# Kernel tuning notes

Measured on AMD Instinct MI355X. Metric: run time of the kernel, lower is better.

The kernel has to match this reference:

```python
import jax, jax.numpy as jnp
import numpy as np
import math

N_HEADS = 16

def _layernorm(x, g, b):
    m = x.mean(-1, keepdims=True)
    v = ((x - m) ** 2).mean(-1, keepdims=True)
    return (x - m) * jax.lax.rsqrt(v + 1e-5) * g + b

def _project(x):
    # Poincare ball (c=1) projection: clip last-dim norm to 1 - eps
    max_norm = 1.0 - 1e-5
    n = jnp.linalg.norm(x, axis=-1, keepdims=True)
    return jnp.where(n > max_norm, x * (max_norm / jnp.maximum(n, 1e-12)), x)


def setup_inputs() -> dict:
    key = jax.random.key(0)
    ks = jax.random.split(key, 8)
    B, L, D = 2, 2048, 1024
    w = lambda k, s: jax.random.normal(k, s, jnp.float32) * 0.02
    return dict(
        x=jax.random.normal(ks[0], (B, L, D), jnp.float32),
        wq=w(ks[1], (D, D)), bq=jnp.zeros((D,), jnp.float32),
        wk=w(ks[2], (D, D)), bk=jnp.zeros((D,), jnp.float32),
        wv=w(ks[3], (D, D)), bv=jnp.zeros((D,), jnp.float32),
        wo=w(ks[4], (D, D)), bo=jnp.zeros((D,), jnp.float32),
        g1=jnp.ones((D,), jnp.float32), b1=jnp.zeros((D,), jnp.float32),
        g2=jnp.ones((D,), jnp.float32), b2=jnp.zeros((D,), jnp.float32),
        w1=w(ks[5], (4 * D, D)), bf1=jnp.zeros((4 * D,), jnp.float32),
        w2=w(ks[6], (D, 4 * D)), bf2=jnp.zeros((D,), jnp.float32),
    )


def reference(x, wq, bq, wk, bk, wv, bv, wo, bo, g1, b1, g2, b2, w1, bf1, w2, bf2):
    B, L, D = x.shape
    H = N_HEADS
    hd = D // H
    temp = math.sqrt(hd)

    xn = _layernorm(x, g1, b1)

    def heads(w, b):
        y = xn @ w.T + b                       # [B, L, D]
        return y.reshape(B, L, H, hd).transpose(0, 2, 1, 3)  # [B, H, L, hd]

    q = _project(heads(wq, bq))
    k = _project(heads(wk, bk))
    v = heads(wv, bv)

    # -||q - k||^2 / temp, via ||q||^2 + ||k||^2 - 2 q.k (same math as the
    # explicit broadcast-diff in the torch code, expressed as a GEMM)
    q2 = (q ** 2).sum(-1)[..., :, None]        # [B, H, L, 1]
    k2 = (k ** 2).sum(-1)[..., None, :]        # [B, H, 1, L]
    qk = jnp.einsum('bhld,bhmd->bhlm', q, k)   # [B, H, L, L]
    scores = -(q2 + k2 - 2.0 * qk) / temp
    attn = jax.nn.softmax(scores, axis=-1)     # dropout = identity (eval mode)

    out = jnp.einsum('bhlm,bhmd->bhld', attn, v)
    out = out.transpose(0, 2, 1, 3).reshape(B, L, D) @ wo.T + bo

    x = _project(x + out)
    xn2 = _layernorm(x, g2, b2)
    h = jax.nn.gelu(xn2 @ w1.T + bf1, approximate=False)  # torch nn.GELU = erf
    x = _project(x + (h @ w2.T + bf2))
    return x
```

## Files before the change

kernel.cpp:

```cpp
#include <hip/hip_runtime.h>
#include <math.h>

#define SEQ_L 2048
#define DM    1024
#define NH    16
#define HD    64
#define BL    4096
#define DFF   4096
#define QKV_S 3072

typedef __attribute__((ext_vector_type(8))) short short8;
typedef __attribute__((ext_vector_type(4))) short s16x4;
typedef __attribute__((ext_vector_type(4))) float f32x4;

#define AS1 __attribute__((address_space(1)))
#define AS3 __attribute__((address_space(3)))

__device__ __forceinline__ void gl_lds16(const void* g, void* l) {
    __builtin_amdgcn_global_load_lds((const AS1 void*)g, (AS3 void*)l, 16, 0, 0);
}

__device__ __forceinline__ short f2bf(float x) {
    unsigned u = __float_as_uint(x);
    u += 0x7fff + ((u >> 16) & 1);
    return (short)(u >> 16);
}
__device__ __forceinline__ float bf2f(short s) {
    return __uint_as_float(((unsigned)(unsigned short)s) << 16);
}

__device__ __forceinline__ float gelu_erf(float x) {
    return 0.5f * x * (1.f + erff(x * 0.70710678118654752440f));
}

__device__ __forceinline__ float block_sum(float v, float* red, int tid) {
#pragma unroll
    for (int m = 32; m; m >>= 1) v += __shfl_xor(v, m);
    if ((tid & 63) == 0) red[tid >> 6] = v;
    __syncthreads();
    v = red[0] + red[1] + red[2] + red[3];
    __syncthreads();
    return v;
}

__global__ __launch_bounds__(256) void cvt6_kernel(
    const float* __restrict__ wq, const float* __restrict__ wk,
    const float* __restrict__ wv, const float* __restrict__ wo,
    const float* __restrict__ w1, const float* __restrict__ w2,
    short* __restrict__ dst) {
    const size_t i = (size_t)blockIdx.x * 256 + threadIdx.x;
    const float* src;
    size_t off;
    if (i < 1048576) {
        const int seg = (int)(i >> 18);
        off = i & 262143;
        src = seg == 0 ? wq : seg == 1 ? wk : seg == 2 ? wv : wo;
    } else if (i < 2097152) { src = w1; off = i - 1048576; }
    else                    { src = w2; off = i - 2097152; }
    const float4 v = ((const float4*)src)[off];
    const s16x4 o = {f2bf(v.x), f2bf(v.y), f2bf(v.z), f2bf(v.w)};
    ((s16x4*)dst)[i] = o;
}

__global__ __launch_bounds__(256) void ln_bf16_kernel(const float* __restrict__ x,
                                                      const float* __restrict__ g,
                                                      const float* __restrict__ b,
                                                      short* __restrict__ out) {
    const int row = blockIdx.x;
    const int tid = threadIdx.x;
    __shared__ float red[4];
    const float4 xv = *(const float4*)(x + (size_t)row * DM + tid * 4);
    float s = xv.x + xv.y + xv.z + xv.w;
    s = block_sum(s, red, tid);
    const float mean = s * (1.f / (float)DM);
    float dx0 = xv.x - mean, dx1 = xv.y - mean, dx2 = xv.z - mean, dx3 = xv.w - mean;
    float ss = dx0 * dx0 + dx1 * dx1 + dx2 * dx2 + dx3 * dx3;
    ss = block_sum(ss, red, tid);
    const float rs = 1.f / sqrtf(ss * (1.f / (float)DM) + 1e-5f);
    const float4 gv = *(const float4*)(g + tid * 4);
    const float4 bv = *(const float4*)(b + tid * 4);
    const s16x4 ob = {f2bf(dx0 * rs * gv.x + bv.x), f2bf(dx1 * rs * gv.y + bv.y),
                      f2bf(dx2 * rs * gv.z + bv.z), f2bf(dx3 * rs * gv.w + bv.w)};
    *(s16x4*)(out + (size_t)row * DM + tid * 4) = ob;
}

__global__ __launch_bounds__(256) void resproj_kernel(const float* __restrict__ a,
                                                      const float* __restrict__ c,
                                                      float* __restrict__ out) {
    const int row = blockIdx.x;
    const int tid = threadIdx.x;
    __shared__ float red[4];
    const float4 av = *(const float4*)(a + (size_t)row * DM + tid * 4);
    const float4 cv = *(const float4*)(c + (size_t)row * DM + tid * 4);
    float4 sv;
    sv.x = av.x + cv.x; sv.y = av.y + cv.y; sv.z = av.z + cv.z; sv.w = av.w + cv.w;
    float ss = sv.x * sv.x + sv.y * sv.y + sv.z * sv.z + sv.w * sv.w;
    ss = block_sum(ss, red, tid);
    const float n = sqrtf(ss);
    const float mx = 1.f - 1e-5f;
    const float scale = (n > mx) ? (mx / fmaxf(n, 1e-12f)) : 1.f;
    sv.x *= scale; sv.y *= scale; sv.z *= scale; sv.w *= scale;
    *(float4*)(out + (size_t)row * DM + tid * 4) = sv;
}

__global__ __launch_bounds__(256) void qk_prep(const short* __restrict__ qkvB,
                                               short* __restrict__ Qb,
                                               short* __restrict__ Kb,
                                               float* __restrict__ k2) {
    const int tid = threadIdx.x, lane = tid & 63;
    const int vec = blockIdx.x * 4 + (tid >> 6);
    const int row = vec >> 4, h = vec & 15;
    const int b = row >> 11, l = row & 2047;
    const size_t dstv = ((size_t)(b * NH + h) * SEQ_L + l) * HD + lane;
    const float mx = 1.f - 1e-5f;
    {
        const float v = bf2f(qkvB[(size_t)row * QKV_S + h * HD + lane]);
        float s = v * v;
#pragma unroll
        for (int m = 32; m; m >>= 1) s += __shfl_xor(s, m);
        const float n = sqrtf(s);
        const float sc = (n > mx) ? (mx / fmaxf(n, 1e-12f)) : 1.f;
        Qb[dstv] = f2bf(v * sc);
    }
    {
        const float v = bf2f(qkvB[(size_t)row * QKV_S + DM + h * HD + lane]);
        float s = v * v;
#pragma unroll
        for (int m = 32; m; m >>= 1) s += __shfl_xor(s, m);
        const float n = sqrtf(s);
        const float sc = (n > mx) ? (mx / fmaxf(n, 1e-12f)) : 1.f;
        Kb[dstv] = f2bf(v * sc);
        if (lane == 0) k2[(size_t)(b * NH + h) * SEQ_L + l] = s * sc * sc * 0.125f;
    }
}

__global__ __launch_bounds__(256) void v_prep(const short* __restrict__ qkvB,
                                              short* __restrict__ Vtb) {
    const int blk = blockIdx.x;
    const int bh = blk >> 5, kt = blk & 31;
    const int b = bh >> 4, h = bh & 15;
    __shared__ short T[64 * 72];
    const int tid = threadIdx.x;
    {
        const int key = tid >> 2, ch = (tid & 3) * 16;
        const size_t src = ((size_t)b * SEQ_L + kt * 64 + key) * QKV_S + 2 * DM + h * HD + ch;
        *(short8*)&T[key * 72 + ch]     = *(const short8*)(qkvB + src);
        *(short8*)&T[key * 72 + ch + 8] = *(const short8*)(qkvB + src + 8);
    }
    __syncthreads();
    const int hd = tid >> 2, kc = (tid & 3) * 16;
    short8 o0, o1;
#pragma unroll
    for (int j = 0; j < 8; ++j) {
        o0[j] = T[(kc + j) * 72 + hd];
        o1[j] = T[(kc + 8 + j) * 72 + hd];
    }
    short* dst = Vtb + ((size_t)bh * HD + hd) * SEQ_L + kt * 64 + kc;
    *(short8*)dst = o0;
    *(short8*)(dst + 8) = o1;
}

template <int BM, int ACT, int OUTBF, int FUSED>
__global__ __launch_bounds__(256) void gemm_mfma(
    const short* __restrict__ A, const short* __restrict__ Bw,
    const float* __restrict__ bb0, const float* __restrict__ bb1,
    const float* __restrict__ bb2, void* __restrict__ Cout,
    int M, int N, int K) {
    constexpr int RT = BM / 32;
    __shared__ __align__(16) short As[BM * 32];
    __shared__ __align__(16) short Bs[128 * 32];
    const int tid = threadIdx.x;
    const int wv = tid >> 6, lane = tid & 63;
    const int m0 = blockIdx.y * BM, n0 = blockIdx.x * 128;
    const int wr = (wv & 1) * (BM / 2);
    const int wc = (wv >> 1) * 64;

    const int arow = wv * (BM / 4) + (lane >> 2);
    const int brow = wv * 32 + (lane >> 2);
    const short* Ag = A + (size_t)(m0 + arow) * K + (lane & 3) * 8;
    const short* Bg = Bw + (size_t)(n0 + brow) * K + (lane & 3) * 8;
    short* AsW = As + (wv * (BM / 4)) * 32;
    short* BsW = Bs + (wv * 32) * 32;

    const f32x4 z4 = {0.f, 0.f, 0.f, 0.f};
    f32x4 acc[RT][4];
#pragma unroll
    for (int r = 0; r < RT; ++r)
#pragma unroll
        for (int c = 0; c < 4; ++c) acc[r][c] = z4;

    const int lrow = lane & 15, kq = (lane >> 4) * 8;

    for (int kt = 0; kt < K; kt += 32) {
        __syncthreads();
        gl_lds16(Ag + kt, AsW);
        if constexpr (BM == 128) gl_lds16(Ag + (size_t)16 * K + kt, AsW + 16 * 32);
        gl_lds16(Bg + kt, BsW);
        gl_lds16(Bg + (size_t)16 * K + kt, BsW + 16 * 32);
        __syncthreads();
        short8 af[RT], bf[4];
#pragma unroll
        for (int r = 0; r < RT; ++r)
            af[r] = *(const short8*)&As[(wr + r * 16 + lrow) * 32 + kq];
#pragma unroll
        for (int c = 0; c < 4; ++c)
            bf[c] = *(const short8*)&Bs[(wc + c * 16 + lrow) * 32 + kq];
#pragma unroll
        for (int r = 0; r < RT; ++r)
#pragma unroll
            for (int c = 0; c < 4; ++c)
                acc[r][c] = __builtin_amdgcn_mfma_f32_16x16x32_bf16(af[r], bf[c], acc[r][c], 0, 0, 0);
    }

    const int col = lane & 15, rb = (lane >> 4) * 4;
#pragma unroll
    for (int c = 0; c < 4; ++c) {
        const int gn = n0 + wc + c * 16 + col;
        float bias;
        if constexpr (FUSED) {
            const int seg = gn >> 10;
            bias = (seg == 0 ? bb0 : seg == 1 ? bb1 : bb2)[gn & 1023];
        } else {
            bias = bb0[gn];
        }
#pragma unroll
        for (int r = 0; r < RT; ++r) {
            const int gm = m0 + wr + r * 16 + rb;
#pragma unroll
            for (int i = 0; i < 4; ++i) {
                float v = acc[r][c][i] + bias;
                if constexpr (ACT) v = gelu_erf(v);
                if constexpr (OUTBF)
                    ((short*)Cout)[(size_t)(gm + i) * N + gn] = f2bf(v);
                else
                    ((float*)Cout)[(size_t)(gm + i) * N + gn] = v;
            }
        }
    }
}

__global__ __launch_bounds__(256) void attn_mfma2(const short* __restrict__ Qb,
                                                  const short* __restrict__ Kb,
                                                  const short* __restrict__ Vtb,
                                                  const float* __restrict__ k2v,
                                                  short* __restrict__ aO) {
    const int qt = blockIdx.x, h = blockIdx.y, b = blockIdx.z;
    const int tid = threadIdx.x, wv = tid >> 6, lane = tid & 63;
    const int bh = b * NH + h;
    __shared__ __align__(16) short smem[2 * 64 * 72];
    short* Ks = smem;
    short* Vt = smem + 64 * 72;
    const int lrow = lane & 15, q8 = (lane >> 4) * 8, q4 = (lane >> 4) * 4;

    const short* Qh = Qb + (size_t)bh * SEQ_L * HD;
    const short* Kh = Kb + (size_t)bh * SEQ_L * HD;
    const short* Vh = Vtb + (size_t)bh * HD * SEQ_L;
    const float* k2p = k2v + (size_t)bh * SEQ_L;

    short8 qf[2][2];
#pragma unroll
    for (int nt = 0; nt < 2; ++nt)
#pragma unroll
        for (int kc = 0; kc < 2; ++kc)
            qf[nt][kc] = *(const short8*)(Qh +
                (size_t)(qt * 128 + wv * 32 + nt * 16 + lrow) * HD + kc * 32 + q8);

    const f32x4 z4 = {0.f, 0.f, 0.f, 0.f};
    f32x4 o[4][2];
#pragma unroll
    for (int ht = 0; ht < 4; ++ht)
#pragma unroll
        for (int nt = 0; nt < 2; ++nt) o[ht][nt] = z4;
    float lsum[2] = {0.f, 0.f};

    const int srow = tid >> 2, sch = (tid & 3) * 16;

    for (int kt = 0; kt < SEQ_L / 64; ++kt) {
        const int k0 = kt * 64;
        __syncthreads();
        {
            const short* g = Kh + (size_t)(k0 + srow) * HD + sch;
            *(short8*)&Ks[srow * 72 + sch]     = *(const short8*)g;
            *(short8*)&Ks[srow * 72 + sch + 8] = *(const short8*)(g + 8);
            const short* gv = Vh + (size_t)srow * SEQ_L + k0 + sch;
            *(short8*)&Vt[srow * 72 + sch]     = *(const short8*)gv;
            *(short8*)&Vt[srow * 72 + sch + 8] = *(const short8*)(gv + 8);
        }
        __syncthreads();

        short8 p8[2][2];
#pragma unroll
        for (int mt = 0; mt < 4; ++mt) {
            const short8 kf0 = *(const short8*)&Ks[(mt * 16 + lrow) * 72 + q8];
            const short8 kf1 = *(const short8*)&Ks[(mt * 16 + lrow) * 72 + 32 + q8];
            const float4 kk = *(const float4*)(k2p + k0 + mt * 16 + q4);
            const int c = mt >> 1, hi = (mt & 1) * 4;
#pragma unroll
            for (int nt = 0; nt < 2; ++nt) {
                f32x4 s = z4;
                s = __builtin_amdgcn_mfma_f32_16x16x32_bf16(kf0, qf[nt][0], s, 0, 0, 0);
                s = __builtin_amdgcn_mfma_f32_16x16x32_bf16(kf1, qf[nt][1], s, 0, 0, 0);
#pragma unroll
                for (int i = 0; i < 4; ++i) {
                    const float kki = (i == 0) ? kk.x : (i == 1) ? kk.y : (i == 2) ? kk.z : kk.w;
                    const float p = __expf(fmaf(s[i], 0.25f, -kki));
                    lsum[nt] += p;
                    p8[nt][c][hi + i] = f2bf(p);
                }
            }
        }
#pragma unroll
        for (int ht = 0; ht < 4; ++ht) {
#pragma unroll
            for (int c = 0; c < 2; ++c) {
                const s16x4 va = *(const s16x4*)&Vt[(ht * 16 + lrow) * 72 + c * 32 + q4];
                const s16x4 vb = *(const s16x4*)&Vt[(ht * 16 + lrow) * 72 + c * 32 + 16 + q4];
                const short8 v8 = {va[0], va[1], va[2], va[3], vb[0], vb[1], vb[2], vb[3]};
#pragma unroll
                for (int nt = 0; nt < 2; ++nt)
                    o[ht][nt] = __builtin_amdgcn_mfma_f32_16x16x32_bf16(v8, p8[nt][c], o[ht][nt], 0, 0, 0);
            }
        }
    }

#pragma unroll
    for (int nt = 0; nt < 2; ++nt) {
        lsum[nt] += __shfl_xor(lsum[nt], 16);
        lsum[nt] += __shfl_xor(lsum[nt], 32);
    }
    const float inv0 = 1.f / lsum[0], inv1 = 1.f / lsum[1];

    __syncthreads();
    short* Ot = smem + wv * (32 * 72);
#pragma unroll
    for (int ht = 0; ht < 4; ++ht)
#pragma unroll
        for (int nt = 0; nt < 2; ++nt) {
            const float iv = nt ? inv1 : inv0;
            const s16x4 ov = {f2bf(o[ht][nt][0] * iv), f2bf(o[ht][nt][1] * iv),
                              f2bf(o[ht][nt][2] * iv), f2bf(o[ht][nt][3] * iv)};
            *(s16x4*)&Ot[(nt * 16 + lrow) * 72 + ht * 16 + q4] = ov;
        }
    const int erow = lane >> 1, ec = (lane & 1) * 32;
    const short8 r0 = *(const short8*)&Ot[erow * 72 + ec + 0];
    const short8 r1 = *(const short8*)&Ot[erow * 72 + ec + 8];
    const short8 r2 = *(const short8*)&Ot[erow * 72 + ec + 16];
    const short8 r3 = *(const short8*)&Ot[erow * 72 + ec + 24];
    short* dst = aO + ((size_t)b * SEQ_L + qt * 128 + wv * 32 + erow) * DM + h * HD + ec;
    *(short8*)(dst + 0)  = r0;
    *(short8*)(dst + 8)  = r1;
    *(short8*)(dst + 16) = r2;
    *(short8*)(dst + 24) = r3;
}

extern "C" void kernel_launch(void* const* d_in, const int* in_sizes, int n_in,
                              void* d_out, int out_size, void* d_ws, size_t ws_size,
                              hipStream_t stream) {
    const float* x   = (const float*)d_in[0];
    const float* wq  = (const float*)d_in[1];
    const float* bq  = (const float*)d_in[2];
    const float* wk  = (const float*)d_in[3];
    const float* bk  = (const float*)d_in[4];
    const float* wv  = (const float*)d_in[5];
    const float* bv  = (const float*)d_in[6];
    const float* wo  = (const float*)d_in[7];
    const float* bo  = (const float*)d_in[8];
    const float* g1  = (const float*)d_in[9];
    const float* b1  = (const float*)d_in[10];
    const float* g2  = (const float*)d_in[11];
    const float* b2  = (const float*)d_in[12];
    const float* w1  = (const float*)d_in[13];
    const float* bf1 = (const float*)d_in[14];
    const float* w2  = (const float*)d_in[15];
    const float* bf2 = (const float*)d_in[16];
    float* out = (float*)d_out;

    char* base = (char*)d_ws;
    short* wbf  = (short*)base;
    short* qkvB = (short*)(base + (24u << 20));
    short* xnb  = (short*)(base + (48u << 20));
    short* Qb   = xnb;
    short* Kb   = (short*)(base + (56u << 20));
    short* Vtb  = (short*)(base + (64u << 20));
    float* k2   = (float*)(base + (72u << 20));
    short* aO   = (short*)(base + (72u << 20) + (256u << 10));
    float* P    = (float*)(base + (24u << 20));
    short* xn2b = Vtb;
    short* hbuf = qkvB;
    float* y2   = (float*)(base + (56u << 20));

    cvt6_kernel<<<12288, 256, 0, stream>>>(wq, wk, wv, wo, w1, w2, wbf);
    ln_bf16_kernel<<<BL, 256, 0, stream>>>(x, g1, b1, xnb);
    gemm_mfma<128, 0, 1, 1><<<dim3(24, 32), 256, 0, stream>>>(
        xnb, wbf, bq, bk, bv, qkvB, BL, QKV_S, DM);
    qk_prep<<<16384, 256, 0, stream>>>(qkvB, Qb, Kb, k2);
    v_prep<<<1024, 256, 0, stream>>>(qkvB, Vtb);
    attn_mfma2<<<dim3(16, 16, 2), 256, 0, stream>>>(Qb, Kb, Vtb, k2, aO);
    gemm_mfma<64, 0, 0, 0><<<dim3(8, 64), 256, 0, stream>>>(
        aO, wbf + 3145728, bo, bo, bo, P, BL, DM, DM);
    resproj_kernel<<<BL, 256, 0, stream>>>(x, P, out);
    ln_bf16_kernel<<<BL, 256, 0, stream>>>(out, g2, b2, xn2b);
    gemm_mfma<128, 1, 1, 0><<<dim3(32, 32), 256, 0, stream>>>(
        xn2b, wbf + 4194304, bf1, bf1, bf1, hbuf, BL, DFF, DM);
    gemm_mfma<64, 0, 0, 0><<<dim3(8, 64), 256, 0, stream>>>(
        hbuf, wbf + 8388608, bf2, bf2, bf2, y2, BL, DM, DFF);
    resproj_kernel<<<BL, 256, 0, stream>>>(out, y2, out);
}
```

Baseline: 438.2 us.

## Stage bf16 GEMM epilogue through LDS for vector stores and use fast GELU

```diff
diff --git a/kernel.cpp b/kernel.cpp
--- a/kernel.cpp
+++ b/kernel.cpp
@@ -29,8 +29,18 @@
     return __uint_as_float(((unsigned)(unsigned short)s) << 16);
 }
 
-__device__ __forceinline__ float gelu_erf(float x) {
-    return 0.5f * x * (1.f + erff(x * 0.70710678118654752440f));
+__device__ __forceinline__ float gelu_fast(float x) {
+    const float xa = fabsf(x);
+    const float z = xa * 0.70710678118654752440f;
+    const float t = __builtin_amdgcn_rcpf(fmaf(0.3275911f, z, 1.f));
+    float P = fmaf(t, 1.061405429f, -1.453152027f);
+    P = fmaf(t, P, 1.421413741f);
+    P = fmaf(t, P, -0.284496736f);
+    P = fmaf(t, P, 0.254829592f);
+    P *= t;
+    const float e = __expf(-z * z);
+    const float erfp = fmaf(-P, e, 1.f);
+    return 0.5f * fmaf(xa, erfp, x);
 }
 
 __device__ __forceinline__ float block_sum(float v, float* red, int tid) {
@@ -167,8 +177,11 @@
     const float* __restrict__ bb2, void* __restrict__ Cout,
     int M, int N, int K) {
     constexpr int RT = BM / 32;
-    __shared__ __align__(16) short As[BM * 32];
-    __shared__ __align__(16) short Bs[128 * 32];
+    constexpr bool VEPI = (OUTBF != 0) && (BM == 128);
+    constexpr int SMEM_BYTES = VEPI ? (4 * 64 * 72 * 2) : ((BM * 32 + 128 * 32) * 2);
+    __shared__ __align__(16) char raw[SMEM_BYTES];
+    short* As = (short*)raw;
+    short* Bs = As + BM * 32;
     const int tid = threadIdx.x;
     const int wv = tid >> 6, lane = tid & 63;
     const int m0 = blockIdx.y * BM, n0 = blockIdx.x * 128;
@@ -213,27 +226,57 @@
     }
 
     const int col = lane & 15, rb = (lane >> 4) * 4;
-#pragma unroll
-    for (int c = 0; c < 4; ++c) {
-        const int gn = n0 + wc + c * 16 + col;
-        float bias;
-        if constexpr (FUSED) {
-            const int seg = gn >> 10;
-            bias = (seg == 0 ? bb0 : seg == 1 ? bb1 : bb2)[gn & 1023];
-        } else {
-            bias = bb0[gn];
-        }
-#pragma unroll
-        for (int r = 0; r < RT; ++r) {
-            const int gm = m0 + wr + r * 16 + rb;
-#pragma unroll
-            for (int i = 0; i < 4; ++i) {
-                float v = acc[r][c][i] + bias;
-                if constexpr (ACT) v = gelu_erf(v);
-                if constexpr (OUTBF)
-                    ((short*)Cout)[(size_t)(gm + i) * N + gn] = f2bf(v);
-                else
-                    ((float*)Cout)[(size_t)(gm + i) * N + gn] = v;
+    if constexpr (VEPI) {
+        __syncthreads();
+        short* Ot = (short*)raw + wv * (64 * 72);
+#pragma unroll
+        for (int c = 0; c < 4; ++c) {
+            const int gn = n0 + wc + c * 16 + col;
+            float bias;
+            if constexpr (FUSED) {
+                const int seg = gn >> 10;
+                bias = (seg == 0 ? bb0 : seg == 1 ? bb1 : bb2)[gn & 1023];
+            } else {
+                bias = bb0[gn];
+            }
+#pragma unroll
+            for (int r = 0; r < RT; ++r)
+#pragma unroll
+                for (int i = 0; i < 4; ++i) {
+                    float v = acc[r][c][i] + bias;
+                    if constexpr (ACT) v = gelu_fast(v);
+                    Ot[(r * 16 + rb + i) * 72 + c * 16 + col] = f2bf(v);
+                }
+        }
+        const int orow = lane >> 3, oc = (lane & 7) * 8;
+#pragma unroll
+        for (int it = 0; it < 8; ++it) {
+            const short8 vv = *(const short8*)&Ot[(it * 8 + orow) * 72 + oc];
+            *(short8*)((short*)Cout + (size_t)(m0 + wr + it * 8 + orow) * N + n0 + wc + oc) = vv;
+        }
+    } else {
+#pragma unroll
+        for (int c = 0; c < 4; ++c) {
+            const int gn = n0 + wc + c * 16 + col;
+            float bias;
+            if constexpr (FUSED) {
+                const int seg = gn >> 10;
+                bias = (seg == 0 ? bb0 : seg == 1 ? bb1 : bb2)[gn & 1023];
+            } else {
+                bias = bb0[gn];
+            }
+#pragma unroll
+            for (int r = 0; r < RT; ++r) {
+                const int gm = m0 + wr + r * 16 + rb;
+#pragma unroll
+                for (int i = 0; i < 4; ++i) {
+                    float v = acc[r][c][i] + bias;
+                    if constexpr (ACT) v = gelu_fast(v);
+                    if constexpr (OUTBF)
+                        ((short*)Cout)[(size_t)(gm + i) * N + gn] = f2bf(v);
+                    else
+                        ((float*)Cout)[(size_t)(gm + i) * N + gn] = v;
+                }
             }
         }
     }
```

New measurement: 426.6 us. -2.6%, faster.
